# Kernel tuning notes

Hardware: AMD Instinct MI355X
Metric: run time of the kernel (lower is better)

The kernel has to match this reference:

```python
import jax, jax.numpy as jnp
import numpy as np

HEAD_DIM = 256
NUM_HEADS = 8
NUM_KV = 1
MAX_WAVELENGTH = 10000.0


def _apply_rope(x, positions):
    # x: [B, S, N, H], positions: [B, S] int
    d = x.shape[-1]
    freq_exponents = (2.0 / d) * jnp.arange(d // 2, dtype=jnp.float32)
    timescale = MAX_WAVELENGTH ** freq_exponents  # [H/2]
    radians = positions[..., None].astype(jnp.float32) / timescale  # [B, S, H/2]
    radians = radians[..., None, :]  # [B, S, 1, H/2]
    sin, cos = jnp.sin(radians), jnp.cos(radians)
    first, second = jnp.split(x.astype(jnp.float32), 2, axis=-1)
    out = jnp.concatenate([first * cos - second * sin, second * cos + first * sin], axis=-1)
    return out.astype(x.dtype)


def setup_inputs() -> dict:
    key = jax.random.key(0)
    ks = jax.random.split(key, 8)
    B, S0, S1 = 4, 768, 256
    W0, W1 = 2048, 1024
    T = S0 + S1
    s = 0.02  # param init scale
    x0 = jax.random.normal(ks[0], (B, S0, W0), jnp.float32)
    x1 = jax.random.normal(ks[1], (B, S1, W1), jnp.float32)
    w_q0 = jax.random.normal(ks[2], (NUM_HEADS, W0, HEAD_DIM), jnp.float32) * s
    w_kv0 = jax.random.normal(ks[3], (2, NUM_KV, W0, HEAD_DIM), jnp.float32) * s
    w_out0 = jax.random.normal(ks[4], (NUM_HEADS, HEAD_DIM, W0), jnp.float32) * s
    w_q1 = jax.random.normal(ks[5], (NUM_HEADS, W1, HEAD_DIM), jnp.float32) * s
    w_kv1 = jax.random.normal(ks[6], (2, NUM_KV, W1, HEAD_DIM), jnp.float32) * s
    w_out1 = jax.random.normal(ks[7], (NUM_HEADS, HEAD_DIM, W1), jnp.float32) * s
    positions = jnp.broadcast_to(jnp.arange(T, dtype=jnp.int32), (B, T))
    attn_mask = jnp.broadcast_to(jnp.tril(jnp.ones((T, T), bool))[None, None], (B, 1, T, T))
    return {"x0": x0, "x1": x1, "w_q0": w_q0, "w_kv0": w_kv0, "w_out0": w_out0,
            "w_q1": w_q1, "w_kv1": w_kv1, "w_out1": w_out1,
            "positions": positions, "attn_mask": attn_mask}


def reference(x0, x1, w_q0, w_kv0, w_out0, w_q1, w_kv1, w_out1, positions, attn_mask):
    dtype = x0.dtype
    # GQA projections per stream (num_kv_heads != num_heads path)
    q0 = jnp.einsum('BTD,NDH->BTNH', x0, w_q0)
    k0, v0 = jnp.einsum('BSD,CKDH->CBSKH', x0, w_kv0)
    q1 = jnp.einsum('BTD,NDH->BTNH', x1, w_q1)
    k1, v1 = jnp.einsum('BSD,CKDH->CBSKH', x1, w_kv1)
    q = jnp.concatenate([q0, q1], axis=1)  # [B, T, N, H]
    k = jnp.concatenate([k0, k1], axis=1)  # [B, T, K, H]
    v = jnp.concatenate([v0, v1], axis=1)
    q = _apply_rope(q, positions) * (HEAD_DIM ** -0.5)
    k = _apply_rope(k, positions)
    B, T = q.shape[0], q.shape[1]
    G = NUM_HEADS // NUM_KV
    q = q.reshape(B, T, NUM_KV, G, HEAD_DIM)
    logits = jnp.einsum('BTKGH,BSKH->BKGTS', q, k, preferred_element_type=jnp.float32)
    big_neg = -2.3819763e38
    masked = jnp.where(attn_mask[:, :, None, :, :], logits, big_neg)
    probs = jax.nn.softmax(masked, axis=-1).astype(dtype)
    encoded = jnp.einsum('BKGTS,BSKH->BTKGH', probs, v).reshape(B, T, NUM_HEADS, HEAD_DIM)
    S0 = x0.shape[1]
    out0 = jnp.einsum('BTNH,NHD->BTD', encoded[:, :S0], w_out0)
    out1 = jnp.einsum('BTNH,NHD->BTD', encoded[:, S0:], w_out1)
    return (out0, out1, k, v)
```

## Files before the change

### kernel.cpp

```cpp
#include <hip/hip_runtime.h>
#include <hip/hip_bf16.h>

typedef __attribute__((ext_vector_type(8))) short bf16x8;
typedef __attribute__((ext_vector_type(4))) float f32x4;
typedef __attribute__((ext_vector_type(4))) unsigned short u16x4;
typedef unsigned short US;

__device__ __forceinline__ f32x4 mfma16(bf16x8 a, bf16x8 b, f32x4 c) {
  return __builtin_amdgcn_mfma_f32_16x16x32_bf16(a, b, c, 0, 0, 0);
}

__device__ __forceinline__ US f2bf(float f) {
  union { float f; unsigned u; } x; x.f = f;
  unsigned r = x.u + 0x7fffu + ((x.u >> 16) & 1u);
  return (US)(r >> 16);
}

__device__ __forceinline__ void gld16(const US* gp, US* lp) {
  __builtin_amdgcn_global_load_lds(
      (const __attribute__((address_space(1))) unsigned*)gp,
      (__attribute__((address_space(3))) unsigned*)lp, 16, 0, 0);
}

__device__ __forceinline__ int permq(int h) {
  return ((h >> 5) << 6) + (h & 15) + (((h >> 4) & 1) << 5);
}

__device__ __forceinline__ int map_row(int r, int mode) {
  if (mode == 1) { int b = r / 768; return b * 1024 + (r - b * 768); }
  if (mode == 2) { int b = r >> 8; return b * 1024 + 768 + (r & 255); }
  return r;
}

__global__ __launch_bounds__(256)
void k_prep(const float* __restrict__ x0, const float* __restrict__ x1,
            US* __restrict__ x0b, US* __restrict__ x1b,
            const float* __restrict__ wq0, const float* __restrict__ wkv0,
            const float* __restrict__ wq1, const float* __restrict__ wkv1,
            US* __restrict__ btq0, US* __restrict__ btkv0,
            US* __restrict__ btq1, US* __restrict__ btkv1,
            const int* __restrict__ pos, float2* __restrict__ sct) {
  const int bid = blockIdx.x;
  const int tid = threadIdx.x;
  if (bid >= 14848) {
    int idx = (bid - 14848) * 256 + tid;
    int bt = idx >> 7, j = idx & 127;
    float inv_ts = __expf(-0.0719557841f * (float)j);
    float r = (float)pos[bt] * inv_ts;
    float s, co;
    __sincosf(r, &s, &co);
    sct[idx] = make_float2(s, co);
    return;
  }
  if (bid < 7168) {
    const float* src; US* dst; int i;
    if (bid < 6144) { src = x0; dst = x0b; i = bid * 256 + tid; }
    else            { src = x1; dst = x1b; i = (bid - 6144) * 256 + tid; }
    f32x4 v = *reinterpret_cast<const f32x4*>(src + (size_t)i * 4);
    u16x4 o;
    o[0] = f2bf(v[0]); o[1] = f2bf(v[1]); o[2] = f2bf(v[2]); o[3] = f2bf(v[3]);
    *reinterpret_cast<u16x4*>(dst + (size_t)i * 4) = o;
    return;
  }
  __shared__ float tile[32][33];
  const float* src; US* dst; int R, C, CX, local; long sbs, dbs; bool pq = false;
  if (bid < 11264)      { local = bid - 7168;  src = wq0;  dst = btq0;  R = 2048; C = 256; CX = 8; sbs = 2048L * 256; dbs = 256L * 2048; pq = true; }
  else if (bid < 12288) { local = bid - 11264; src = wkv0; dst = btkv0; R = 2048; C = 256; CX = 8; sbs = 2048L * 256; dbs = 256L * 2048; }
  else if (bid < 14336) { local = bid - 12288; src = wq1;  dst = btq1;  R = 1024; C = 256; CX = 8; sbs = 1024L * 256; dbs = 256L * 1024; pq = true; }
  else                  { local = bid - 14336; src = wkv1; dst = btkv1; R = 1024; C = 256; CX = 8; sbs = 1024L * 256; dbs = 256L * 1024; }
  const int RY = R >> 5;
  const int cx = local % CX;
  const int rest = local / CX;
  const int ry = rest % RY;
  const int z = rest / RY;
  const int c0 = cx * 32, r0 = ry * 32;
  const int tx = tid & 31, ty = tid >> 5;
  src += (long)z * sbs;
  dst += (long)z * dbs;
#pragma unroll
  for (int i = 0; i < 4; ++i)
    tile[ty + 8 * i][tx] = src[(size_t)(r0 + ty + 8 * i) * C + c0 + tx];
  __syncthreads();
#pragma unroll
  for (int i = 0; i < 4; ++i) {
    int h = c0 + ty + 8 * i;
    int ph = pq ? ((h < 128) ? permq(h) : permq(h - 128) + 16) : h;
    dst[(size_t)ph * R + r0 + tx] = f2bf(tile[tx][ty + 8 * i]);
  }
}

__global__ __launch_bounds__(256, 2)
void k_gemm_qkv(const US* __restrict__ x0b, const US* __restrict__ x1b,
                const US* __restrict__ btq0, const US* __restrict__ btq1,
                US* __restrict__ q_bf, float* __restrict__ Ckv,
                const float2* __restrict__ sct) {
  const int bid = blockIdx.x;
  const US* A; const US* BT; int K, cmap, by, bx;
  if (bid < 480) {
    int id = (bid & 7) * 60 + (bid >> 3);
    A = x0b; BT = btq0; K = 2048; cmap = 1; by = id / 20; bx = id % 20;
  } else {
    int l = bid - 480;
    int id = (l & 7) * 20 + (l >> 3);
    A = x1b; BT = btq1; K = 1024; cmap = 2; by = id / 20; bx = id % 20;
  }

  __shared__ __align__(16) US lA[2][128 * 32];
  __shared__ __align__(16) US lB[2][128 * 32];
  const int tid = threadIdx.x;
  const int lane = tid & 63;
  const int wid = tid >> 6;
  const int wm = wid >> 1, wn = wid & 1;
  const int m0 = by * 128, n0 = bx * 128;
  const int g = lane >> 4, c = lane & 15;
  const int lrow = lane >> 2, lcol = (lane & 3) * 8;
  const size_t ga0 = (size_t)(m0 + wid * 16 + lrow) * K + lcol;
  const size_t ga1 = (size_t)(m0 + 64 + wid * 16 + lrow) * K + lcol;
  const size_t gb0 = (size_t)(n0 + wid * 16 + lrow) * K + lcol;
  const size_t gb1 = (size_t)(n0 + 64 + wid * 16 + lrow) * K + lcol;

  auto stage = [&](int bi, int k0) {
    gld16(A + ga0 + k0, &lA[bi][(wid * 16) * 32]);
    gld16(A + ga1 + k0, &lA[bi][(64 + wid * 16) * 32]);
    gld16(BT + gb0 + k0, &lB[bi][(wid * 16) * 32]);
    gld16(BT + gb1 + k0, &lB[bi][(64 + wid * 16) * 32]);
  };

  f32x4 acc[4][4];
#pragma unroll
  for (int i = 0; i < 4; ++i)
#pragma unroll
    for (int j = 0; j < 4; ++j) acc[i][j] = f32x4{0.f, 0.f, 0.f, 0.f};

  const int nt = K >> 5;
  stage(0, 0);
  __syncthreads();
  for (int t = 0; t < nt; ++t) {
    const int bi = t & 1;
    if (t + 1 < nt) stage(bi ^ 1, (t + 1) * 32);
    bf16x8 af[4], bfr[4];
#pragma unroll
    for (int i = 0; i < 4; ++i) {
      af[i] = *reinterpret_cast<const bf16x8*>(&lA[bi][(wm * 64 + i * 16 + c) * 32 + g * 8]);
      bfr[i] = *reinterpret_cast<const bf16x8*>(&lB[bi][(wn * 64 + i * 16 + c) * 32 + g * 8]);
    }
#pragma unroll
    for (int i = 0; i < 4; ++i)
#pragma unroll
      for (int j = 0; j < 4; ++j)
        acc[i][j] = mfma16(af[i], bfr[j], acc[i][j]);
    __syncthreads();
  }

  const int colb = n0 + wn * 64;
  if (colb < 2048) {
    const int n = colb >> 8;
    const int base64 = colb & 255;
    const int h0 = (base64 >> 6) * 32 + c;
    const float scale = 0.0625f;
#pragma unroll
    for (int i = 0; i < 4; ++i) {
#pragma unroll
      for (int r = 0; r < 4; ++r) {
        const int orow = map_row(m0 + wm * 64 + i * 16 + 4 * g + r, cmap);
        const float2 sc0 = sct[orow * 128 + h0];
        const float2 sc1 = sct[orow * 128 + h0 + 16];
        US* qp = q_bf + ((size_t)orow * 8 + n) * 256 + base64 + c;
        const float q1 = acc[i][0][r], q2 = acc[i][1][r];
        const float q3 = acc[i][2][r], q4 = acc[i][3][r];
        qp[0]  = f2bf(scale * (q1 * sc0.y - q2 * sc0.x));
        qp[16] = f2bf(scale * (q2 * sc0.y + q1 * sc0.x));
        qp[32] = f2bf(scale * (q3 * sc1.y - q4 * sc1.x));
        qp[48] = f2bf(scale * (q4 * sc1.y + q3 * sc1.x));
      }
    }
  } else {
    const int nb = colb - 2048 + c;
#pragma unroll
    for (int i = 0; i < 4; ++i) {
#pragma unroll
      for (int r = 0; r < 4; ++r) {
        const int orow = map_row(m0 + wm * 64 + i * 16 + 4 * g + r, cmap);
        float* cp = Ckv + (size_t)orow * 512 + nb;
#pragma unroll
        for (int j = 0; j < 4; ++j) cp[j * 16] = acc[i][j][r];
      }
    }
  }
}

__global__ __launch_bounds__(256, 2)
void k_gemm_out(const US* __restrict__ A, const US* __restrict__ BT0, const US* __restrict__ BT1,
                float* __restrict__ C0, float* __restrict__ C1) {
  const int bid = blockIdx.x;
  int id = (bid & 7) * 56 + (bid >> 3);
  const US* BT; float* Cb; int amap, mt, ntile, Nst;
  if (id < 384) { amap = 1; mt = id / 16; ntile = id % 16; BT = BT0; Cb = C0; Nst = 2048; }
  else { id -= 384; amap = 2; mt = id / 8; ntile = id % 8; BT = BT1; Cb = C1; Nst = 1024; }
  const int m0 = mt * 128, n0 = ntile * 128;
  const int K = 2048;
  __shared__ __align__(16) US lA[2][128 * 32];
  __shared__ __align__(16) US lB[2][128 * 32];
  const int tid = threadIdx.x;
  const int lane = tid & 63;
  const int wid = tid >> 6;
  const int wm = wid >> 1, wn = wid & 1;
  const int g = lane >> 4, c = lane & 15;
  const int lrow = lane >> 2, lcol = (lane & 3) * 8;
  const size_t ga0 = (size_t)map_row(m0 + wid * 16 + lrow, amap) * K + lcol;
  const size_t ga1 = (size_t)map_row(m0 + 64 + wid * 16 + lrow, amap) * K + lcol;
  const size_t gb0 = (size_t)(n0 + wid * 16 + lrow) * K + lcol;
  const size_t gb1 = (size_t)(n0 + 64 + wid * 16 + lrow) * K + lcol;

  auto stage = [&](int bi, int k0) {
    gld16(A + ga0 + k0, &lA[bi][(wid * 16) * 32]);
    gld16(A + ga1 + k0, &lA[bi][(64 + wid * 16) * 32]);
    gld16(BT + gb0 + k0, &lB[bi][(wid * 16) * 32]);
    gld16(BT + gb1 + k0, &lB[bi][(64 + wid * 16) * 32]);
  };

  f32x4 acc[4][4];
#pragma unroll
  for (int i = 0; i < 4; ++i)
#pragma unroll
    for (int j = 0; j < 4; ++j) acc[i][j] = f32x4{0.f, 0.f, 0.f, 0.f};

  const int nt = K >> 5;
  stage(0, 0);
  __syncthreads();
  for (int t = 0; t < nt; ++t) {
    const int bi = t & 1;
    if (t + 1 < nt) stage(bi ^ 1, (t + 1) * 32);
    bf16x8 af[4], bfr[4];
#pragma unroll
    for (int i = 0; i < 4; ++i) {
      af[i] = *reinterpret_cast<const bf16x8*>(&lA[bi][(wm * 64 + i * 16 + c) * 32 + g * 8]);
      bfr[i] = *reinterpret_cast<const bf16x8*>(&lB[bi][(wn * 64 + i * 16 + c) * 32 + g * 8]);
    }
#pragma unroll
    for (int i = 0; i < 4; ++i)
#pragma unroll
      for (int j = 0; j < 4; ++j)
        acc[i][j] = mfma16(af[i], bfr[j], acc[i][j]);
    __syncthreads();
  }

  const int col = n0 + wn * 64 + c;
#pragma unroll
  for (int i = 0; i < 4; ++i) {
#pragma unroll
    for (int r = 0; r < 4; ++r) {
      const int orow = m0 + wm * 64 + i * 16 + 4 * g + r;
      float* cp = Cb + (size_t)orow * Nst + col;
#pragma unroll
      for (int j = 0; j < 4; ++j) cp[j * 16] = acc[i][j][r];
    }
  }
}

__global__ __launch_bounds__(256)
void k_postkv(const float* __restrict__ kv_raw, const float2* __restrict__ sct,
              US* __restrict__ k_bf, float* __restrict__ k_out,
              float* __restrict__ v_out, US* __restrict__ vt) {
  const int bid = blockIdx.x;
  const int tid = threadIdx.x;
  if (bid >= 1024) {
    const int bt = (bid - 1024) * 2 + (tid >> 7);
    const int j = tid & 127;
    const size_t ko = (size_t)bt * 512;
    const float x1 = kv_raw[ko + j], x2 = kv_raw[ko + j + 128];
    const float2 sc = sct[bt * 128 + j];
    const float o1 = x1 * sc.y - x2 * sc.x, o2 = x2 * sc.y + x1 * sc.x;
    const size_t kd = (size_t)bt * 256;
    const int p = permq(j);
    k_bf[kd + p] = f2bf(o1);
    k_bf[kd + p + 16] = f2bf(o2);
    k_out[kd + j] = o1;
    k_out[kd + j + 128] = o2;
    return;
  }
  __shared__ float tile[32][33];
  const int t0 = (bid & 31) * 32, h0 = ((bid >> 5) & 7) * 32, b = bid >> 8;
  const int tx = tid & 31, ty = tid >> 5;
#pragma unroll
  for (int i = 0; i < 4; ++i) {
    int t = t0 + ty + 8 * i;
    float v = kv_raw[(size_t)(b * 1024 + t) * 512 + 256 + h0 + tx];
    tile[ty + 8 * i][tx] = v;
    v_out[(size_t)(b * 1024 + t) * 256 + h0 + tx] = v;
  }
  __syncthreads();
#pragma unroll
  for (int i = 0; i < 4; ++i) {
    int h = h0 + ty + 8 * i;
    vt[(size_t)(b * 256 + h) * 1024 + t0 + tx] = f2bf(tile[tx][ty + 8 * i]);
  }
}

__global__ __launch_bounds__(256, 2)
void k_attn(const US* __restrict__ qb, const US* __restrict__ kb,
            const US* __restrict__ vt, US* __restrict__ enc,
            const float* __restrict__ wo0, const float* __restrict__ wo1,
            US* __restrict__ bto0, US* __restrict__ bto1) {
  __shared__ __align__(16) US lK[2][32 * 256];
  __shared__ __align__(16) US lV[2][256 * 32];
  const int id = blockIdx.x;
  const int tid = threadIdx.x;

  if (id >= 512) {
    int local = id - 512;
    const float* src; US* dst; int C, CX;
    if (local < 4096) { src = wo0; dst = bto0; C = 2048; CX = 64; }
    else { local -= 4096; src = wo1; dst = bto1; C = 1024; CX = 32; }
    const int cx = local % CX, ry = local / CX;
    const int c0p = cx * 32, r0p = ry * 32;
    const int tx = tid & 31, ty = tid >> 5;
    float* tileF = (float*)&lK[0][0];
#pragma unroll
    for (int i = 0; i < 4; ++i)
      tileF[(ty + 8 * i) * 33 + tx] = src[(size_t)(r0p + ty + 8 * i) * C + c0p + tx];
    __syncthreads();
#pragma unroll
    for (int i = 0; i < 4; ++i)
      dst[(size_t)(c0p + ty + 8 * i) * 2048 + r0p + tx] = f2bf(tileF[tx * 33 + ty + 8 * i]);
    return;
  }

  const int r0_ = (id < 256) ? id : 767 - id;
  const int qt = 63 - (r0_ >> 3);
  const int hg = (r0_ >> 2) & 1;
  const int b = r0_ & 3;
  const int wid = tid >> 6;
  const int lane = tid & 63;
  const int g = lane >> 4, c = lane & 15;
  const int qbase = qt * 16;
  const int n = hg * 4 + wid;

  const US* kbB = kb + (size_t)b * 262144;
  const US* vtB = vt + (size_t)b * 262144;

  bf16x8 qf[8];
  {
    const US* qp = qb + ((size_t)((b * 1024 + qbase + c) * 8 + n)) * 256 + 8 * g;
#pragma unroll
    for (int ch = 0; ch < 8; ++ch)
      qf[ch] = *reinterpret_cast<const bf16x8*>(qp + ch * 32);
  }

  auto stage = [&](int bi, int c0) {
#pragma unroll
    for (int j = 0; j < 4; ++j) {
      const int rk = wid * 8 + j * 2 + (lane >> 5);
      const int sk = lane & 31;
      gld16(kbB + (size_t)(c0 + rk) * 256 + (sk ^ (rk & 7)) * 8,
            &lK[bi][(wid * 8 + j * 2) * 256]);
      const int rv = wid * 64 + j * 16 + (lane >> 2);
      const int sv = lane & 3;
      gld16(vtB + (size_t)rv * 1024 + c0 + (sv ^ ((rv >> 1) & 3)) * 8,
            &lV[bi][(wid * 64 + j * 16) * 32]);
    }
  };

  f32x4 acc[16];
#pragma unroll
  for (int i = 0; i < 16; ++i) acc[i] = f32x4{0.f, 0.f, 0.f, 0.f};
  float m_run = -3.0e38f, l_run = 0.f;

  const int nC = qbase / 32 + 1;
  stage(0, 0);
  __syncthreads();

  for (int i = 0; i < nC; ++i) {
    const int c0 = 32 * i;
    const int bi = i & 1;
    if (i + 1 < nC) stage(bi ^ 1, c0 + 32);

    const bool hb = (c0 + 16 <= qbase);
    f32x4 sA = {0.f, 0.f, 0.f, 0.f}, sB = {0.f, 0.f, 0.f, 0.f};
    __builtin_amdgcn_s_setprio(1);
#pragma unroll
    for (int ch = 0; ch < 8; ++ch) {
      const int slot = (((ch * 4 + g) ^ (c & 7)) * 8);
      sA = mfma16(*reinterpret_cast<const bf16x8*>(&lK[bi][c * 256 + slot]), qf[ch], sA);
    }
    if (hb) {
#pragma unroll
      for (int ch = 0; ch < 8; ++ch) {
        const int slot = (((ch * 4 + g) ^ (c & 7)) * 8);
        sB = mfma16(*reinterpret_cast<const bf16x8*>(&lK[bi][(c + 16) * 256 + slot]), qf[ch], sB);
      }
    }
    __builtin_amdgcn_s_setprio(0);
    if (c0 == qbase) {
#pragma unroll
      for (int r = 0; r < 4; ++r)
        if (4 * g + r > c) sA[r] = -3.0e38f;
    }
    if (hb && (c0 + 16 == qbase)) {
#pragma unroll
      for (int r = 0; r < 4; ++r)
        if (4 * g + r > c) sB[r] = -3.0e38f;
    }
    float tm = fmaxf(fmaxf(sA[0], sA[1]), fmaxf(sA[2], sA[3]));
    if (hb) tm = fmaxf(tm, fmaxf(fmaxf(sB[0], sB[1]), fmaxf(sB[2], sB[3])));
    tm = fmaxf(tm, __shfl_xor(tm, 16));
    tm = fmaxf(tm, __shfl_xor(tm, 32));
    if (!__all(tm - m_run <= 8.0f)) {
      const float m_new = fmaxf(m_run, tm);
      const float alpha = __expf(m_run - m_new);
      float aacc[4];
#pragma unroll
      for (int r = 0; r < 4; ++r) aacc[r] = __shfl(alpha, 4 * g + r);
#pragma unroll
      for (int ht = 0; ht < 16; ++ht) {
        acc[ht][0] *= aacc[0]; acc[ht][1] *= aacc[1];
        acc[ht][2] *= aacc[2]; acc[ht][3] *= aacc[3];
      }
      l_run *= alpha;
      m_run = m_new;
    }
    float pA[4], pB[4];
    float ls = 0.f;
#pragma unroll
    for (int r = 0; r < 4; ++r) { pA[r] = __expf(sA[r] - m_run); ls += pA[r]; }
#pragma unroll
    for (int r = 0; r < 4; ++r) { pB[r] = hb ? __expf(sB[r] - m_run) : 0.f; ls += pB[r]; }
    ls += __shfl_xor(ls, 16);
    ls += __shfl_xor(ls, 32);
    l_run += ls;

    unsigned w0, w1, w2, w3;
    asm("v_cvt_pk_bf16_f32 %0, %1, %2" : "=v"(w0) : "v"(pA[0]), "v"(pA[1]));
    asm("v_cvt_pk_bf16_f32 %0, %1, %2" : "=v"(w1) : "v"(pA[2]), "v"(pA[3]));
    asm("v_cvt_pk_bf16_f32 %0, %1, %2" : "=v"(w2) : "v"(pB[0]), "v"(pB[1]));
    asm("v_cvt_pk_bf16_f32 %0, %1, %2" : "=v"(w3) : "v"(pB[2]), "v"(pB[3]));
    const bool bb1 = ((g >> 1) & 1) != 0, bb0 = (g & 1) != 0;
    unsigned ownA = bb1 ? w2 : w0, ownB = bb1 ? w3 : w1;
    unsigned sndA = bb1 ? w0 : w2, sndB = bb1 ? w1 : w3;
    unsigned rcvA = (unsigned)__shfl_xor((int)sndA, 32);
    unsigned rcvB = (unsigned)__shfl_xor((int)sndB, 32);
    unsigned kA = (bb0 == bb1) ? ownA : rcvA, kB = (bb0 == bb1) ? ownB : rcvB;
    unsigned s2A = (bb0 == bb1) ? rcvA : ownA, s2B = (bb0 == bb1) ? rcvB : ownB;
    unsigned gA = (unsigned)__shfl_xor((int)s2A, 16);
    unsigned gB = (unsigned)__shfl_xor((int)s2B, 16);
    union { unsigned u[4]; bf16x8 v; } pu;
    pu.u[0] = bb0 ? gA : kA; pu.u[1] = bb0 ? gB : kB;
    pu.u[2] = bb0 ? kA : gA; pu.u[3] = bb0 ? kB : gB;
    const bf16x8 paf = pu.v;

    __builtin_amdgcn_s_setprio(1);
#pragma unroll
    for (int ht = 0; ht < 16; ++ht) {
      const int h = ht * 16 + c;
      const int slot = (g ^ ((c >> 1) & 3)) * 8;
      bf16x8 vf = *reinterpret_cast<const bf16x8*>(&lV[bi][h * 32 + slot]);
      acc[ht] = mfma16(paf, vf, acc[ht]);
    }
    __builtin_amdgcn_s_setprio(0);
    __syncthreads();
  }

  const float inv = 1.0f / l_run;
  float ia[4];
#pragma unroll
  for (int r = 0; r < 4; ++r) ia[r] = __shfl(inv, 4 * g + r);
#pragma unroll
  for (int ht = 0; ht < 16; ++ht) {
#pragma unroll
    for (int r = 0; r < 4; ++r) {
      size_t o = ((size_t)((b * 1024 + qbase + 4 * g + r) * 8 + n)) * 256 + ht * 16 + c;
      enc[o] = f2bf(acc[ht][r] * ia[r]);
    }
  }
}

extern "C" void kernel_launch(void* const* d_in, const int* in_sizes, int n_in,
                              void* d_out, int out_size, void* d_ws, size_t ws_size,
                              hipStream_t stream) {
  const float* x0 = (const float*)d_in[0];
  const float* x1 = (const float*)d_in[1];
  const float* wq0 = (const float*)d_in[2];
  const float* wkv0 = (const float*)d_in[3];
  const float* wo0 = (const float*)d_in[4];
  const float* wq1 = (const float*)d_in[5];
  const float* wkv1 = (const float*)d_in[6];
  const float* wo1 = (const float*)d_in[7];
  const int* pos = (const int*)d_in[8];
  float* out = (float*)d_out;

  float* out0 = out;
  float* out1 = out + 6291456;
  float* k_out = out + 7340032;
  float* v_out = out + 8388608;

  char* ws = (char*)d_ws;
  size_t off = 0;
  auto alloc = [&](size_t bytes) {
    char* p = ws + off;
    off += (bytes + 255) & ~(size_t)255;
    return p;
  };
  US* x0b   = (US*)alloc(6291456ull * 2);
  US* x1b   = (US*)alloc(1048576ull * 2);
  US* btq0  = (US*)alloc(2048ull * 2048 * 2);
  US* btkv0 = (US*)alloc(512ull * 2048 * 2);
  US* btq1  = (US*)alloc(2048ull * 1024 * 2);
  US* btkv1 = (US*)alloc(512ull * 1024 * 2);
  US* bto0  = (US*)alloc(2048ull * 2048 * 2);
  US* bto1  = (US*)alloc(1024ull * 2048 * 2);
  float* kv_raw = (float*)alloc(2097152ull * 4);
  US* q_bf = (US*)alloc(8388608ull * 2);
  US* k_bf = (US*)alloc(1048576ull * 2);
  US* vt   = (US*)alloc(1048576ull * 2 + 256);
  US* enc  = (US*)alloc(8388608ull * 2);
  float2* sct = (float2*)alloc(524288ull * 8);
  (void)btkv0; (void)btkv1;

  k_prep<<<16896, 256, 0, stream>>>(x0, x1, x0b, x1b, wq0, wkv0, wq1, wkv1,
                                    btq0, btkv0, btq1, btkv1, pos, sct);

  k_gemm_qkv<<<640, 256, 0, stream>>>(x0b, x1b, btq0, btq1, q_bf, kv_raw, sct);

  k_postkv<<<3072, 256, 0, stream>>>(kv_raw, sct, k_bf, k_out, v_out, vt);

  k_attn<<<6656, 256, 0, stream>>>(q_bf, k_bf, vt, enc, wo0, wo1, bto0, bto1);

  k_gemm_out<<<448, 256, 0, stream>>>(enc, bto0, bto1, out0, out1);
}
```

Measured before the change: 186.8 us.

## Fuse K RoPE and V transpose into QKV GEMM epilogue, drop postkv kernel

Removes the separate k_postkv kernel and the fp32 kv_raw intermediate buffer. The QKV GEMM epilogue now applies RoPE to K, writing both bf16 permuted K and fp32 k_out, and writes V both as fp32 output and as a transposed bf16 buffer. The K weight columns are permuted during prep so the epilogue can pair the RoPE halves the same way it does for Q. This saves one kernel launch and a round trip through global memory, at the cost of heavier, less coalesced scattered stores in the GEMM epilogue.

After: 182.9 us. 2.1% less time.

```diff
diff --git a/kernel.cpp b/kernel.cpp
--- a/kernel.cpp
+++ b/kernel.cpp
@@ -63,11 +63,12 @@
     return;
   }
   __shared__ float tile[32][33];
-  const float* src; US* dst; int R, C, CX, local; long sbs, dbs; bool pq = false;
+  const float* src; US* dst; int R, C, CX, local; long sbs, dbs;
+  bool pq = false, pkv = false;
   if (bid < 11264)      { local = bid - 7168;  src = wq0;  dst = btq0;  R = 2048; C = 256; CX = 8; sbs = 2048L * 256; dbs = 256L * 2048; pq = true; }
-  else if (bid < 12288) { local = bid - 11264; src = wkv0; dst = btkv0; R = 2048; C = 256; CX = 8; sbs = 2048L * 256; dbs = 256L * 2048; }
+  else if (bid < 12288) { local = bid - 11264; src = wkv0; dst = btkv0; R = 2048; C = 256; CX = 8; sbs = 2048L * 256; dbs = 256L * 2048; pkv = true; }
   else if (bid < 14336) { local = bid - 12288; src = wq1;  dst = btq1;  R = 1024; C = 256; CX = 8; sbs = 1024L * 256; dbs = 256L * 1024; pq = true; }
-  else                  { local = bid - 14336; src = wkv1; dst = btkv1; R = 1024; C = 256; CX = 8; sbs = 1024L * 256; dbs = 256L * 1024; }
+  else                  { local = bid - 14336; src = wkv1; dst = btkv1; R = 1024; C = 256; CX = 8; sbs = 1024L * 256; dbs = 256L * 1024; pkv = true; }
   const int RY = R >> 5;
   const int cx = local % CX;
   const int rest = local / CX;
@@ -77,6 +78,7 @@
   const int tx = tid & 31, ty = tid >> 5;
   src += (long)z * sbs;
   dst += (long)z * dbs;
+  const bool doperm = pq || (pkv && z == 0);
 #pragma unroll
   for (int i = 0; i < 4; ++i)
     tile[ty + 8 * i][tx] = src[(size_t)(r0 + ty + 8 * i) * C + c0 + tx];
@@ -84,7 +86,7 @@
 #pragma unroll
   for (int i = 0; i < 4; ++i) {
     int h = c0 + ty + 8 * i;
-    int ph = pq ? ((h < 128) ? permq(h) : permq(h - 128) + 16) : h;
+    int ph = doperm ? ((h < 128) ? permq(h) : permq(h - 128) + 16) : h;
     dst[(size_t)ph * R + r0 + tx] = f2bf(tile[tx][ty + 8 * i]);
   }
 }
@@ -92,8 +94,9 @@
 __global__ __launch_bounds__(256, 2)
 void k_gemm_qkv(const US* __restrict__ x0b, const US* __restrict__ x1b,
                 const US* __restrict__ btq0, const US* __restrict__ btq1,
-                US* __restrict__ q_bf, float* __restrict__ Ckv,
-                const float2* __restrict__ sct) {
+                US* __restrict__ q_bf, US* __restrict__ k_bf,
+                float* __restrict__ k_out, float* __restrict__ v_out,
+                US* __restrict__ vt, const float2* __restrict__ sct) {
   const int bid = blockIdx.x;
   const US* A; const US* BT; int K, cmap, by, bx;
   if (bid < 480) {
@@ -174,16 +177,46 @@
         qp[48] = f2bf(scale * (q4 * sc1.y + q3 * sc1.x));
       }
     }
-  } else {
-    const int nb = colb - 2048 + c;
+  } else if (colb < 2304) {
+    const int pcb = colb - 2048;
+    const int h0 = (pcb >> 6) * 32 + c;
 #pragma unroll
     for (int i = 0; i < 4; ++i) {
 #pragma unroll
       for (int r = 0; r < 4; ++r) {
         const int orow = map_row(m0 + wm * 64 + i * 16 + 4 * g + r, cmap);
-        float* cp = Ckv + (size_t)orow * 512 + nb;
-#pragma unroll
-        for (int j = 0; j < 4; ++j) cp[j * 16] = acc[i][j][r];
+        const float2 sc0 = sct[orow * 128 + h0];
+        const float2 sc1 = sct[orow * 128 + h0 + 16];
+        const float q1 = acc[i][0][r], q2 = acc[i][1][r];
+        const float q3 = acc[i][2][r], q4 = acc[i][3][r];
+        const float o1 = q1 * sc0.y - q2 * sc0.x, o2 = q2 * sc0.y + q1 * sc0.x;
+        const float o3 = q3 * sc1.y - q4 * sc1.x, o4 = q4 * sc1.y + q3 * sc1.x;
+        US* kp = k_bf + (size_t)orow * 256 + pcb + c;
+        kp[0] = f2bf(o1); kp[16] = f2bf(o2); kp[32] = f2bf(o3); kp[48] = f2bf(o4);
+        float* ko = k_out + (size_t)orow * 256;
+        ko[h0] = o1; ko[h0 + 128] = o2; ko[h0 + 16] = o3; ko[h0 + 144] = o4;
+      }
+    }
+  } else {
+    const int vcb = colb - 2304 + c;
+#pragma unroll
+    for (int i = 0; i < 4; ++i) {
+#pragma unroll
+      for (int r = 0; r < 4; ++r) {
+        const int orow = map_row(m0 + wm * 64 + i * 16 + 4 * g + r, cmap);
+        float* vo = v_out + (size_t)orow * 256 + vcb;
+#pragma unroll
+        for (int j = 0; j < 4; ++j) vo[j * 16] = acc[i][j][r];
+      }
+      const int orow0 = map_row(m0 + wm * 64 + i * 16 + 4 * g, cmap);
+      const int bb = orow0 >> 10, tt = orow0 & 1023;
+#pragma unroll
+      for (int j = 0; j < 4; ++j) {
+        const int h = vcb + j * 16;
+        u16x4 o;
+        o[0] = f2bf(acc[i][j][0]); o[1] = f2bf(acc[i][j][1]);
+        o[2] = f2bf(acc[i][j][2]); o[3] = f2bf(acc[i][j][3]);
+        *reinterpret_cast<u16x4*>(vt + ((size_t)(bb * 256 + h)) * 1024 + tt) = o;
       }
     }
   }
@@ -258,45 +291,6 @@
   }
 }
 
-__global__ __launch_bounds__(256)
-void k_postkv(const float* __restrict__ kv_raw, const float2* __restrict__ sct,
-              US* __restrict__ k_bf, float* __restrict__ k_out,
-              float* __restrict__ v_out, US* __restrict__ vt) {
-  const int bid = blockIdx.x;
-  const int tid = threadIdx.x;
-  if (bid >= 1024) {
-    const int bt = (bid - 1024) * 2 + (tid >> 7);
-    const int j = tid & 127;
-    const size_t ko = (size_t)bt * 512;
-    const float x1 = kv_raw[ko + j], x2 = kv_raw[ko + j + 128];
-    const float2 sc = sct[bt * 128 + j];
-    const float o1 = x1 * sc.y - x2 * sc.x, o2 = x2 * sc.y + x1 * sc.x;
-    const size_t kd = (size_t)bt * 256;
-    const int p = permq(j);
-    k_bf[kd + p] = f2bf(o1);
-    k_bf[kd + p + 16] = f2bf(o2);
-    k_out[kd + j] = o1;
-    k_out[kd + j + 128] = o2;
-    return;
-  }
-  __shared__ float tile[32][33];
-  const int t0 = (bid & 31) * 32, h0 = ((bid >> 5) & 7) * 32, b = bid >> 8;
-  const int tx = tid & 31, ty = tid >> 5;
-#pragma unroll
-  for (int i = 0; i < 4; ++i) {
-    int t = t0 + ty + 8 * i;
-    float v = kv_raw[(size_t)(b * 1024 + t) * 512 + 256 + h0 + tx];
-    tile[ty + 8 * i][tx] = v;
-    v_out[(size_t)(b * 1024 + t) * 256 + h0 + tx] = v;
-  }
-  __syncthreads();
-#pragma unroll
-  for (int i = 0; i < 4; ++i) {
-    int h = h0 + ty + 8 * i;
-    vt[(size_t)(b * 256 + h) * 1024 + t0 + tx] = f2bf(tile[tx][ty + 8 * i]);
-  }
-}
-
 __global__ __launch_bounds__(256, 2)
 void k_attn(const US* __restrict__ qb, const US* __restrict__ kb,
             const US* __restrict__ vt, US* __restrict__ enc,
@@ -508,7 +502,6 @@
   US* btkv1 = (US*)alloc(512ull * 1024 * 2);
   US* bto0  = (US*)alloc(2048ull * 2048 * 2);
   US* bto1  = (US*)alloc(1024ull * 2048 * 2);
-  float* kv_raw = (float*)alloc(2097152ull * 4);
   US* q_bf = (US*)alloc(8388608ull * 2);
   US* k_bf = (US*)alloc(1048576ull * 2);
   US* vt   = (US*)alloc(1048576ull * 2 + 256);
@@ -519,9 +512,8 @@
   k_prep<<<16896, 256, 0, stream>>>(x0, x1, x0b, x1b, wq0, wkv0, wq1, wkv1,
                                     btq0, btkv0, btq1, btkv1, pos, sct);
 
-  k_gemm_qkv<<<640, 256, 0, stream>>>(x0b, x1b, btq0, btq1, q_bf, kv_raw, sct);
-
-  k_postkv<<<3072, 256, 0, stream>>>(kv_raw, sct, k_bf, k_out, v_out, vt);
+  k_gemm_qkv<<<640, 256, 0, stream>>>(x0b, x1b, btq0, btq1,
+                                      q_bf, k_bf, k_out, v_out, vt, sct);
 
   k_attn<<<6656, 256, 0, stream>>>(q_bf, k_bf, vt, enc, wo0, wo1, bto0, bto1);
 
```
